# Kernel tuning notes

Measured on AMD Instinct MI355X. Metric: run time of the kernel, lower is better.

Reference implementation:

```python
import jax, jax.numpy as jnp
import numpy as np

HEADS = 8
DIM_HEAD = 64
SCALE = DIM_HEAD ** -0.5


def setup_inputs() -> dict:
    key = jax.random.key(0)
    ks = jax.random.split(key, 6)
    b, n, d = 2, 4096, 1024
    inner = HEADS * DIM_HEAD  # 512
    x = jax.random.normal(ks[0], (b, n, d), dtype=jnp.float32)
    Wq = jax.random.normal(ks[1], (d, inner), dtype=jnp.float32) * (d ** -0.5)
    Wk = jax.random.normal(ks[2], (d, inner), dtype=jnp.float32) * (d ** -0.5)
    Wv = jax.random.normal(ks[3], (d, inner), dtype=jnp.float32) * (d ** -0.5)
    Wout = jax.random.normal(ks[4], (inner, d), dtype=jnp.float32) * (inner ** -0.5)
    bout = jnp.zeros((d,), dtype=jnp.float32)
    return {"x": x, "Wq": Wq, "Wk": Wk, "Wv": Wv, "Wout": Wout, "bout": bout}


def reference(x, Wq, Wk, Wv, Wout, bout):
    b, n, _ = x.shape
    h, dh = HEADS, DIM_HEAD
    # self-attention: context = x
    q = (x @ Wq).reshape(b, n, h, dh).transpose(0, 2, 1, 3)  # b h n d
    k = (x @ Wk).reshape(b, n, h, dh).transpose(0, 2, 1, 3)
    v = (x @ Wv).reshape(b, n, h, dh).transpose(0, 2, 1, 3)
    sim = jnp.einsum('bhid,bhjd->bhij', q, k) * SCALE  # full score matrix
    attn = jax.nn.softmax(sim, axis=-1)
    out = jnp.einsum('bhij,bhjd->bhid', attn, v)
    out = out.transpose(0, 2, 1, 3).reshape(b, n, h * dh)  # b n (h d)
    return out @ Wout + bout
```

## Files before the change

### kernel.cpp

```cpp
#include <hip/hip_runtime.h>
#include <hip/hip_bf16.h>

typedef __bf16 bf16x8 __attribute__((ext_vector_type(8)));
typedef __bf16 bf16x4 __attribute__((ext_vector_type(4)));
typedef float floatx4 __attribute__((ext_vector_type(4)));

#define MFMA16(a, b, c) __builtin_amdgcn_mfma_f32_16x16x32_bf16((a), (b), (c), 0, 0, 0)

__device__ __forceinline__ void stage16(const __bf16* g, __bf16* lds_base) {
  __builtin_amdgcn_global_load_lds(
      (__attribute__((address_space(1))) void*)(void*)g,
      (__attribute__((address_space(3))) void*)lds_base, 16, 0, 0);
}

__global__ void detect_dtype(const unsigned int* __restrict__ x, int* __restrict__ flag) {
  __shared__ int cnt;
  if (threadIdx.x == 0) cnt = 0;
  __syncthreads();
  int c = 0;
  for (int i = threadIdx.x; i < 4096; i += 256) {
    const unsigned f = (x[i] >> 7) & 0xFF;
    c += (f >= 100 && f <= 140) ? 1 : 0;
  }
  atomicAdd(&cnt, c);
  __syncthreads();
  if (threadIdx.x == 0) *flag = (cnt > 2048) ? 1 : 0;
}

__global__ __launch_bounds__(256) void convert_x(const void* __restrict__ src,
                                                 __bf16* __restrict__ dst,
                                                 const int* __restrict__ flagp) {
  const int isbf = *flagp;
  const size_t i = ((size_t)blockIdx.x * 256 + threadIdx.x) * 8;
  if (isbf) {
    *(bf16x8*)(dst + i) = *(const bf16x8*)((const __bf16*)src + i);
  } else {
    const float4 f0 = *(const float4*)((const float*)src + i);
    const float4 f1 = *(const float4*)((const float*)src + i + 4);
    bf16x8 v;
    v[0] = (__bf16)f0.x; v[1] = (__bf16)f0.y; v[2] = (__bf16)f0.z; v[3] = (__bf16)f0.w;
    v[4] = (__bf16)f1.x; v[5] = (__bf16)f1.y; v[6] = (__bf16)f1.z; v[7] = (__bf16)f1.w;
    *(bf16x8*)(dst + i) = v;
  }
}

__global__ __launch_bounds__(256) void transpose3_conv(
    const void* __restrict__ s0, const void* __restrict__ s1,
    const void* __restrict__ s2, __bf16* __restrict__ dst,
    int R, int C, const int* __restrict__ flagp) {
  __shared__ __bf16 t[32][33];
  const int isbf = *flagp;
  const void* src = (blockIdx.z == 0) ? s0 : (blockIdx.z == 1) ? s1 : s2;
  __bf16* d = dst + (size_t)blockIdx.z * R * C;
  const int bx = blockIdx.x * 32, by = blockIdx.y * 32;
  const int x = threadIdx.x & 31, y0 = threadIdx.x >> 5;
#pragma unroll
  for (int i = y0; i < 32; i += 8) {
    const size_t idx = (size_t)(by + i) * C + bx + x;
    t[i][x] = isbf ? ((const __bf16*)src)[idx] : (__bf16)(((const float*)src)[idx]);
  }
  __syncthreads();
#pragma unroll
  for (int i = y0; i < 32; i += 8) d[(size_t)(bx + i) * R + by + x] = t[x][i];
}

__global__ __launch_bounds__(256) void transpose_conv(const void* __restrict__ src,
                                                      __bf16* __restrict__ dst,
                                                      int R, int C,
                                                      const int* __restrict__ flagp) {
  __shared__ __bf16 t[32][33];
  const int isbf = *flagp;
  const int bx = blockIdx.x * 32, by = blockIdx.y * 32;
  const int x = threadIdx.x & 31, y0 = threadIdx.x >> 5;
#pragma unroll
  for (int i = y0; i < 32; i += 8) {
    const size_t idx = (size_t)(by + i) * C + bx + x;
    t[i][x] = isbf ? ((const __bf16*)src)[idx] : (__bf16)(((const float*)src)[idx]);
  }
  __syncthreads();
#pragma unroll
  for (int i = y0; i < 32; i += 8) dst[(size_t)(bx + i) * R + by + x] = t[x][i];
}

__global__ __launch_bounds__(256) void gemm_bt(
    const __bf16* __restrict__ A, const __bf16* __restrict__ Bt,
    void* __restrict__ Cv, void* __restrict__ Cv2, int M, int N, int K,
    const void* __restrict__ bias, int permute, int egress_dual,
    size_t zsC, const int* __restrict__ flagp) {
  __shared__ __attribute__((aligned(16))) __bf16 SH[24576];
  const int isbf = *flagp;
  const int gx = gridDim.x;
  const int nwg = gx * gridDim.y;
  const int orig = blockIdx.x + blockIdx.y * gx;
  const int qq = nwg >> 3;
  const int swz = (orig & 7) * qq + (orig >> 3);
  const int bx = swz % gx, by = swz / gx;

  const int tid = threadIdx.x;
  const int wave = tid >> 6, lane = tid & 63;
  const int m0 = by * 128, n0 = bx * 128;
  const int wm = (wave & 1) * 64, wn = (wave >> 1) * 64;
  const int fr = lane & 15, fq = lane >> 4;

  const floatx4 zero4 = {0.f, 0.f, 0.f, 0.f};
  floatx4 acc[4][4];
#pragma unroll
  for (int i = 0; i < 4; i++)
#pragma unroll
    for (int j = 0; j < 4; j++) acc[i][j] = zero4;

  const int lrow = lane >> 2;
  const int lk = (lane & 3) * 8;
  const int NT = K >> 5;

#pragma unroll
  for (int t0 = 0; t0 < 2; ++t0) {
    const int kk = t0 << 5;
#pragma unroll
    for (int cc = 0; cc < 2; ++cc) {
      const int c = 2 * wave + cc;
      stage16(A + (size_t)(m0 + c * 16 + lrow) * K + kk + lk,
              &SH[t0 * 4096 + c * 512]);
      stage16(Bt + (size_t)(n0 + c * 16 + lrow) * K + kk + lk,
              &SH[12288 + t0 * 4096 + c * 512]);
    }
  }

  for (int t = 0; t < NT; ++t) {
    const int cur = t % 3;
    if (t + 2 < NT) {
      const int sl = (t + 2) % 3;
      const int k2 = (t + 2) << 5;
#pragma unroll
      for (int cc = 0; cc < 2; ++cc) {
        const int c = 2 * wave + cc;
        stage16(A + (size_t)(m0 + c * 16 + lrow) * K + k2 + lk,
                &SH[sl * 4096 + c * 512]);
        stage16(Bt + (size_t)(n0 + c * 16 + lrow) * K + k2 + lk,
                &SH[12288 + sl * 4096 + c * 512]);
      }
      asm volatile("s_waitcnt vmcnt(8)" ::: "memory");
    } else if (t + 1 < NT) {
      asm volatile("s_waitcnt vmcnt(4)" ::: "memory");
    } else {
      asm volatile("s_waitcnt vmcnt(0)" ::: "memory");
    }
    __builtin_amdgcn_s_barrier();
    __builtin_amdgcn_sched_barrier(0);
    bf16x8 af[4], bg[4];
#pragma unroll
    for (int mt = 0; mt < 4; mt++)
      af[mt] = *(const bf16x8*)&SH[cur * 4096 + (wm + mt * 16 + fr) * 32 + fq * 8];
#pragma unroll
    for (int nt = 0; nt < 4; nt++)
      bg[nt] = *(const bf16x8*)&SH[12288 + cur * 4096 + (wn + nt * 16 + fr) * 32 + fq * 8];
#pragma unroll
    for (int mt = 0; mt < 4; mt++)
#pragma unroll
      for (int nt = 0; nt < 4; nt++)
        acc[mt][nt] = MFMA16(af[mt], bg[nt], acc[mt][nt]);
    __builtin_amdgcn_sched_barrier(0);
    __builtin_amdgcn_s_barrier();
  }

  if (permute) {
    const float qs = (n0 < 512) ? 0.18033688011112042f : 1.0f;
#pragma unroll
    for (int mt = 0; mt < 4; mt++)
#pragma unroll
      for (int nt = 0; nt < 4; nt++)
#pragma unroll
        for (int r = 0; r < 4; r++) {
          const int lr = wm + mt * 16 + fq * 4 + r;
          const int lc = wn + nt * 16 + fr;
          SH[lr * 136 + lc] = (__bf16)(acc[mt][nt][r] * qs);
        }
    __syncthreads();
    const int bB = m0 >> 12;
    if (n0 < 1024) {
      const int plane = n0 >> 9;
      const int lr = tid >> 1, ch = (tid & 1) << 6;
      const int col0 = n0 + ch;
      const int bh = bB * 8 + ((col0 & 511) >> 6);
      __bf16* rowp = (__bf16*)Cv + (size_t)plane * zsC + (size_t)bh * 262144 +
                     (size_t)((m0 + lr) & 4095) * 64;
      const __bf16* srcp = &SH[lr * 136 + ch];
#pragma unroll
      for (int k = 0; k < 8; ++k)
        *(bf16x8*)(rowp + k * 8) = *(const bf16x8*)(srcp + k * 8);
    } else {
      const int dloc = tid >> 1, gh = tid & 1;
      const int col0 = n0 + dloc;
      const int bh = bB * 8 + ((col0 & 511) >> 6);
      const int d = col0 & 63;
      __bf16* outp = (__bf16*)Cv2 + (size_t)bh * 262144 + (size_t)d * 4096 +
                     ((m0 & 4095) + (gh << 6));
      const int srow0 = gh << 6;
#pragma unroll
      for (int k = 0; k < 8; ++k) {
        bf16x8 w;
#pragma unroll
        for (int e = 0; e < 8; ++e) {
          const int p = k * 8 + e;
          const int tsrc = ((p & 3) << 4) | (p >> 2);
          w[e] = SH[(srow0 + tsrc) * 136 + dloc];
        }
        *(bf16x8*)(outp + k * 8) = w;
      }
    }
  } else {
#pragma unroll
    for (int mt = 0; mt < 4; mt++)
#pragma unroll
      for (int nt = 0; nt < 4; nt++)
#pragma unroll
        for (int r = 0; r < 4; r++) {
          const int row = m0 + wm + mt * 16 + fq * 4 + r;
          const int col = n0 + wn + nt * 16 + fr;
          float v = acc[mt][nt][r];
          if (bias)
            v += isbf ? (float)((const __bf16*)bias)[col] : ((const float*)bias)[col];
          const size_t idx = (size_t)row * N + col;
          if (egress_dual && !isbf)
            ((float*)Cv)[idx] = v;
          else
            ((__bf16*)Cv)[idx] = (__bf16)v;
        }
  }
}

#define ATT_S 4096
__global__ __launch_bounds__(256, 2) void attn_flash(
    const __bf16* __restrict__ Qa, const __bf16* __restrict__ Ka,
    const __bf16* __restrict__ VPa, __bf16* __restrict__ O) {
  alignas(16) __shared__ __bf16 Kl[3][64 * 64];
  alignas(16) __shared__ __bf16 Vl[3][64 * 64];
  alignas(16) __shared__ __bf16 Pl[4 * 32 * 64];
  const int tid = threadIdx.x, wave = tid >> 6, lane = tid & 63;
  const int orig = blockIdx.x + blockIdx.y * 32;
  const int swz = (orig & 7) * 64 + (orig >> 3);
  const int qx = swz & 31, bh = swz >> 5;
  const int b = bh >> 3, h = bh & 7;
  const int q0 = qx * 128 + wave * 32;
  const int fr = lane & 15, fq = lane >> 4;
  const __bf16* Qb = Qa + (size_t)bh * ATT_S * 64;
  const __bf16* Kb = Ka + (size_t)bh * ATT_S * 64;
  const __bf16* Vb = VPa + (size_t)bh * ATT_S * 64;

  const int sw0 = ((fq ^ (fr & 7)) * 8);
  const int sw1 = (((fq + 4) ^ (fr & 7)) * 8);
  const int r0 = tid >> 3;
  const int ssw = (((tid & 7) ^ (r0 & 7)) * 8);

  bf16x8 aq[2][2];
#pragma unroll
  for (int mt = 0; mt < 2; mt++)
#pragma unroll
    for (int kt = 0; kt < 2; kt++)
      aq[mt][kt] = *(const bf16x8*)(Qb + (size_t)(q0 + mt * 16 + fr) * 64 + kt * 32 + fq * 8);

  const floatx4 zero4 = {0.f, 0.f, 0.f, 0.f};
  floatx4 o[2][4];
  float lsum[2][4];
#pragma unroll
  for (int mt = 0; mt < 2; mt++) {
#pragma unroll
    for (int nt = 0; nt < 4; nt++) o[mt][nt] = zero4;
#pragma unroll
    for (int r = 0; r < 4; r++) lsum[mt][r] = 0.f;
  }

  const int JT = ATT_S / 64;

#pragma unroll
  for (int t0 = 0; t0 < 2; ++t0) {
    const int kv = t0 * 64;
    stage16(Kb + (size_t)(kv + r0) * 64 + ssw, &Kl[t0][wave * 512]);
    stage16(Kb + (size_t)(kv + 32 + r0) * 64 + ssw, &Kl[t0][2048 + wave * 512]);
    stage16(Vb + (size_t)r0 * 4096 + kv + ssw, &Vl[t0][wave * 512]);
    stage16(Vb + (size_t)(32 + r0) * 4096 + kv + ssw, &Vl[t0][2048 + wave * 512]);
  }

  for (int j = 0; j < JT; ++j) {
    const int cur = j % 3;
    if (j + 2 < JT) {
      const int sl = (j + 2) % 3;
      const int kv2 = (j + 2) * 64;
      stage16(Kb + (size_t)(kv2 + r0) * 64 + ssw, &Kl[sl][wave * 512]);
      stage16(Kb + (size_t)(kv2 + 32 + r0) * 64 + ssw, &Kl[sl][2048 + wave * 512]);
      stage16(Vb + (size_t)r0 * 4096 + kv2 + ssw, &Vl[sl][wave * 512]);
      stage16(Vb + (size_t)(32 + r0) * 4096 + kv2 + ssw, &Vl[sl][2048 + wave * 512]);
      asm volatile("s_waitcnt vmcnt(8)" ::: "memory");
    } else if (j + 1 < JT) {
      asm volatile("s_waitcnt vmcnt(4)" ::: "memory");
    } else {
      asm volatile("s_waitcnt vmcnt(0)" ::: "memory");
    }
    __builtin_amdgcn_s_barrier();
    __builtin_amdgcn_sched_barrier(0);
    const __bf16* Klc = Kl[cur];
    const __bf16* Vlc = Vl[cur];

    floatx4 s4[2][4];
    __builtin_amdgcn_s_setprio(1);
#pragma unroll
    for (int nt = 0; nt < 4; nt++) {
      bf16x8 bk0 = *(const bf16x8*)&Klc[(nt * 16 + fr) * 64 + sw0];
      bf16x8 bk1 = *(const bf16x8*)&Klc[(nt * 16 + fr) * 64 + sw1];
#pragma unroll
      for (int mt = 0; mt < 2; mt++) {
        floatx4 zz = zero4;
        zz = MFMA16(aq[mt][0], bk0, zz);
        zz = MFMA16(aq[mt][1], bk1, zz);
        s4[mt][nt] = zz;
      }
    }
    __builtin_amdgcn_s_setprio(0);

#pragma unroll
    for (int mt = 0; mt < 2; mt++)
#pragma unroll
      for (int r = 0; r < 4; r++) {
        bf16x4 pv;
        float psum = 0.f;
#pragma unroll
        for (int nt = 0; nt < 4; nt++) {
          const float p = __builtin_amdgcn_exp2f(s4[mt][nt][r]);
          pv[nt] = (__bf16)p;
          psum += p;
        }
        lsum[mt][r] += psum;
        const int row = wave * 32 + mt * 16 + fq * 4 + r;
        const int vg = (fr >> 1) ^ ((fq * 4 + r) & 7);
        *(bf16x4*)&Pl[row * 64 + vg * 8 + (fr & 1) * 4] = pv;
      }
    asm volatile("s_waitcnt lgkmcnt(0)" ::: "memory");

    bf16x8 bv[4][2];
#pragma unroll
    for (int nt = 0; nt < 4; nt++) {
      bv[nt][0] = *(const bf16x8*)&Vlc[(nt * 16 + fr) * 64 + sw0];
      bv[nt][1] = *(const bf16x8*)&Vlc[(nt * 16 + fr) * 64 + sw1];
    }
    __builtin_amdgcn_s_setprio(1);
#pragma unroll
    for (int mt = 0; mt < 2; mt++) {
      const int prow = (wave * 32 + mt * 16 + fr) * 64;
      bf16x8 ap0 = *(const bf16x8*)&Pl[prow + sw0];
      bf16x8 ap1 = *(const bf16x8*)&Pl[prow + sw1];
#pragma unroll
      for (int nt = 0; nt < 4; nt++) {
        o[mt][nt] = MFMA16(ap0, bv[nt][0], o[mt][nt]);
        o[mt][nt] = MFMA16(ap1, bv[nt][1], o[mt][nt]);
      }
    }
    __builtin_amdgcn_s_setprio(0);
    __builtin_amdgcn_sched_barrier(0);
    __builtin_amdgcn_s_barrier();
  }

#pragma unroll
  for (int off = 1; off < 16; off <<= 1)
#pragma unroll
    for (int mt = 0; mt < 2; mt++)
#pragma unroll
      for (int r = 0; r < 4; r++) lsum[mt][r] += __shfl_xor(lsum[mt][r], off, 64);

#pragma unroll
  for (int mt = 0; mt < 2; mt++)
#pragma unroll
    for (int r = 0; r < 4; r++) {
      const float inv = 1.0f / lsum[mt][r];
      const int row = q0 + mt * 16 + fq * 4 + r;
      __bf16* Orow = O + (size_t)(b * ATT_S + row) * 512 + h * 64;
#pragma unroll
      for (int nt = 0; nt < 4; nt++)
        Orow[nt * 16 + fr] = (__bf16)(o[mt][nt][r] * inv);
    }
}

extern "C" void kernel_launch(void* const* d_in, const int* in_sizes, int n_in,
                              void* d_out, int out_size, void* d_ws, size_t ws_size,
                              hipStream_t stream) {
  (void)in_sizes; (void)n_in; (void)out_size; (void)ws_size;
  const void* x = d_in[0];
  const void* Wq = d_in[1];
  const void* Wk = d_in[2];
  const void* Wv = d_in[3];
  const void* Wout = d_in[4];
  const void* bout = d_in[5];

  char* ws = (char*)d_ws;
  int* flag = (int*)ws;
  __bf16* wtq = (__bf16*)(ws + (1u << 20));
  __bf16* wto = (__bf16*)(ws + (4u << 20));
  __bf16* Q = (__bf16*)(ws + (5u << 20));
  __bf16* K = (__bf16*)(ws + (13u << 20));
  __bf16* VP = (__bf16*)(ws + (21u << 20));
  __bf16* O = (__bf16*)(ws + (29u << 20));
  __bf16* xbf = (__bf16*)(ws + (38u << 20));

  detect_dtype<<<1, 256, 0, stream>>>((const unsigned int*)x, flag);

  transpose3_conv<<<dim3(16, 32, 3), 256, 0, stream>>>(Wq, Wk, Wv, wtq, 1024, 512, flag);
  transpose_conv<<<dim3(32, 16), 256, 0, stream>>>(Wout, wto, 512, 1024, flag);

  convert_x<<<4096, 256, 0, stream>>>(x, xbf, flag);

  gemm_bt<<<dim3(12, 64, 1), 256, 0, stream>>>(
      xbf, wtq, Q, VP, 8192, 1536, 1024, nullptr, 1, 0,
      (size_t)8192 * 512, flag);

  attn_flash<<<dim3(ATT_S / 128, 16), 256, 0, stream>>>(Q, K, VP, O);

  gemm_bt<<<dim3(8, 64, 1), 256, 0, stream>>>(
      O, wto, d_out, nullptr, 8192, 1024, 512, bout, 0, 1, 0, flag);
}
```

Measured before the change: 248.2 us.

## Switch attention to 32x32 MFMA with transposed scores kept in registers

Rewrites the flash-attention inner loop to use 32x32x16 bf16 MFMAs and computes S^T (K as A operand, Q as B operand). The exponentiated probabilities are packed to bf16 and rearranged with cross-half lane shuffles so they can feed the P·V MFMA directly. This removes the P tile's round trip through LDS and its lgkmcnt wait. Row sums are reduced through a small LDS buffer at the end, at the cost of extra packing and shuffle work in registers.

```diff
diff --git a/kernel.cpp b/kernel.cpp
--- a/kernel.cpp
+++ b/kernel.cpp
@@ -4,13 +4,21 @@
 typedef __bf16 bf16x8 __attribute__((ext_vector_type(8)));
 typedef __bf16 bf16x4 __attribute__((ext_vector_type(4)));
 typedef float floatx4 __attribute__((ext_vector_type(4)));
+typedef float floatx16 __attribute__((ext_vector_type(16)));
 
 #define MFMA16(a, b, c) __builtin_amdgcn_mfma_f32_16x16x32_bf16((a), (b), (c), 0, 0, 0)
+#define MFMA32(a, b, c) __builtin_amdgcn_mfma_f32_32x32x16_bf16((a), (b), (c), 0, 0, 0)
 
 __device__ __forceinline__ void stage16(const __bf16* g, __bf16* lds_base) {
   __builtin_amdgcn_global_load_lds(
       (__attribute__((address_space(1))) void*)(void*)g,
       (__attribute__((address_space(3))) void*)lds_base, 16, 0, 0);
+}
+
+__device__ __forceinline__ unsigned pkbf(float lo, float hi) {
+  union { unsigned u; __bf16 h[2]; } w;
+  w.h[0] = (__bf16)lo; w.h[1] = (__bf16)hi;
+  return w.u;
 }
 
 __global__ void detect_dtype(const unsigned int* __restrict__ x, int* __restrict__ flag) {
@@ -235,42 +243,33 @@
     const __bf16* __restrict__ VPa, __bf16* __restrict__ O) {
   alignas(16) __shared__ __bf16 Kl[3][64 * 64];
   alignas(16) __shared__ __bf16 Vl[3][64 * 64];
-  alignas(16) __shared__ __bf16 Pl[4 * 32 * 64];
+  __shared__ float Lw[4][32];
   const int tid = threadIdx.x, wave = tid >> 6, lane = tid & 63;
   const int orig = blockIdx.x + blockIdx.y * 32;
   const int swz = (orig & 7) * 64 + (orig >> 3);
   const int qx = swz & 31, bh = swz >> 5;
   const int b = bh >> 3, h = bh & 7;
   const int q0 = qx * 128 + wave * 32;
-  const int fr = lane & 15, fq = lane >> 4;
+  const int ln = lane & 31, g = lane >> 5;
   const __bf16* Qb = Qa + (size_t)bh * ATT_S * 64;
   const __bf16* Kb = Ka + (size_t)bh * ATT_S * 64;
   const __bf16* Vb = VPa + (size_t)bh * ATT_S * 64;
 
-  const int sw0 = ((fq ^ (fr & 7)) * 8);
-  const int sw1 = (((fq + 4) ^ (fr & 7)) * 8);
   const int r0 = tid >> 3;
   const int ssw = (((tid & 7) ^ (r0 & 7)) * 8);
 
-  bf16x8 aq[2][2];
-#pragma unroll
-  for (int mt = 0; mt < 2; mt++)
-#pragma unroll
-    for (int kt = 0; kt < 2; kt++)
-      aq[mt][kt] = *(const bf16x8*)(Qb + (size_t)(q0 + mt * 16 + fr) * 64 + kt * 32 + fq * 8);
-
-  const floatx4 zero4 = {0.f, 0.f, 0.f, 0.f};
-  floatx4 o[2][4];
-  float lsum[2][4];
-#pragma unroll
-  for (int mt = 0; mt < 2; mt++) {
-#pragma unroll
-    for (int nt = 0; nt < 4; nt++) o[mt][nt] = zero4;
-#pragma unroll
-    for (int r = 0; r < 4; r++) lsum[mt][r] = 0.f;
-  }
+  bf16x8 aq2[4];
+#pragma unroll
+  for (int ds = 0; ds < 4; ds++)
+    aq2[ds] = *(const bf16x8*)(Qb + (size_t)(q0 + ln) * 64 + ds * 16 + g * 8);
+
+  floatx16 o0, o1;
+#pragma unroll
+  for (int r = 0; r < 16; r++) { o0[r] = 0.f; o1[r] = 0.f; }
+  float lsum = 0.f;
 
   const int JT = ATT_S / 64;
+  const int swlo = ln & 7;
 
 #pragma unroll
   for (int t0 = 0; t0 < 2; ++t0) {
@@ -301,82 +300,97 @@
     const __bf16* Klc = Kl[cur];
     const __bf16* Vlc = Vl[cur];
 
-    floatx4 s4[2][4];
+    floatx16 s0, s1;
+#pragma unroll
+    for (int r = 0; r < 16; r++) { s0[r] = 0.f; s1[r] = 0.f; }
     __builtin_amdgcn_s_setprio(1);
 #pragma unroll
-    for (int nt = 0; nt < 4; nt++) {
-      bf16x8 bk0 = *(const bf16x8*)&Klc[(nt * 16 + fr) * 64 + sw0];
-      bf16x8 bk1 = *(const bf16x8*)&Klc[(nt * 16 + fr) * 64 + sw1];
-#pragma unroll
-      for (int mt = 0; mt < 2; mt++) {
-        floatx4 zz = zero4;
-        zz = MFMA16(aq[mt][0], bk0, zz);
-        zz = MFMA16(aq[mt][1], bk1, zz);
-        s4[mt][nt] = zz;
-      }
+    for (int ds = 0; ds < 4; ds++) {
+      const int cg = ds * 2 + g;
+      bf16x8 ak0 = *(const bf16x8*)&Klc[ln * 64 + (cg ^ swlo) * 8];
+      bf16x8 ak1 = *(const bf16x8*)&Klc[(32 + ln) * 64 + (cg ^ swlo) * 8];
+      s0 = MFMA32(ak0, aq2[ds], s0);
+      s1 = MFMA32(ak1, aq2[ds], s1);
     }
     __builtin_amdgcn_s_setprio(0);
 
-#pragma unroll
-    for (int mt = 0; mt < 2; mt++)
-#pragma unroll
-      for (int r = 0; r < 4; r++) {
-        bf16x4 pv;
-        float psum = 0.f;
-#pragma unroll
-        for (int nt = 0; nt < 4; nt++) {
-          const float p = __builtin_amdgcn_exp2f(s4[mt][nt][r]);
-          pv[nt] = (__bf16)p;
-          psum += p;
-        }
-        lsum[mt][r] += psum;
-        const int row = wave * 32 + mt * 16 + fq * 4 + r;
-        const int vg = (fr >> 1) ^ ((fq * 4 + r) & 7);
-        *(bf16x4*)&Pl[row * 64 + vg * 8 + (fr & 1) * 4] = pv;
-      }
-    asm volatile("s_waitcnt lgkmcnt(0)" ::: "memory");
-
-    bf16x8 bv[4][2];
-#pragma unroll
-    for (int nt = 0; nt < 4; nt++) {
-      bv[nt][0] = *(const bf16x8*)&Vlc[(nt * 16 + fr) * 64 + sw0];
-      bv[nt][1] = *(const bf16x8*)&Vlc[(nt * 16 + fr) * 64 + sw1];
-    }
+    float e0[16], e1[16];
+    float ps = 0.f;
+#pragma unroll
+    for (int r = 0; r < 16; r++) {
+      e0[r] = __builtin_amdgcn_exp2f(s0[r]);
+      e1[r] = __builtin_amdgcn_exp2f(s1[r]);
+      ps += e0[r] + e1[r];
+    }
+    lsum += ps;
+
+    unsigned Aw[4] = {pkbf(e0[0], e0[8]),  pkbf(e1[0], e1[8]),
+                      pkbf(e0[1], e0[9]),  pkbf(e1[1], e1[9])};
+    unsigned Bw[4] = {pkbf(e0[2], e0[10]), pkbf(e1[2], e1[10]),
+                      pkbf(e0[3], e0[11]), pkbf(e1[3], e1[11])};
+    unsigned Cw[4] = {pkbf(e0[4], e0[12]), pkbf(e1[4], e1[12]),
+                      pkbf(e0[5], e0[13]), pkbf(e1[5], e1[13])};
+    unsigned Dw[4] = {pkbf(e0[6], e0[14]), pkbf(e1[6], e1[14]),
+                      pkbf(e0[7], e0[15]), pkbf(e1[7], e1[15])};
+    union W8u { unsigned u[4]; bf16x8 v; } fk0, fk1, fk2, fk3;
+#pragma unroll
+    for (int i = 0; i < 4; i++) {
+      const unsigned u1 = g ? Aw[i] : Bw[i];
+      const unsigned r1 = (unsigned)__shfl_xor((int)u1, 32, 64);
+      fk0.u[i] = g ? r1 : Aw[i];
+      fk1.u[i] = g ? Bw[i] : r1;
+      const unsigned u2 = g ? Cw[i] : Dw[i];
+      const unsigned r2 = (unsigned)__shfl_xor((int)u2, 32, 64);
+      fk2.u[i] = g ? r2 : Cw[i];
+      fk3.u[i] = g ? Dw[i] : r2;
+    }
+
     __builtin_amdgcn_s_setprio(1);
-#pragma unroll
-    for (int mt = 0; mt < 2; mt++) {
-      const int prow = (wave * 32 + mt * 16 + fr) * 64;
-      bf16x8 ap0 = *(const bf16x8*)&Pl[prow + sw0];
-      bf16x8 ap1 = *(const bf16x8*)&Pl[prow + sw1];
-#pragma unroll
-      for (int nt = 0; nt < 4; nt++) {
-        o[mt][nt] = MFMA16(ap0, bv[nt][0], o[mt][nt]);
-        o[mt][nt] = MFMA16(ap1, bv[nt][1], o[mt][nt]);
-      }
+    {
+      const int vr = ln;
+      bf16x8 bv0 = *(const bf16x8*)&Vlc[vr * 64 + ((0 + g) ^ swlo) * 8];
+      bf16x8 bv1 = *(const bf16x8*)&Vlc[vr * 64 + ((2 + g) ^ swlo) * 8];
+      bf16x8 bv2 = *(const bf16x8*)&Vlc[vr * 64 + ((4 + g) ^ swlo) * 8];
+      bf16x8 bv3 = *(const bf16x8*)&Vlc[vr * 64 + ((6 + g) ^ swlo) * 8];
+      o0 = MFMA32(fk0.v, bv0, o0);
+      o0 = MFMA32(fk1.v, bv1, o0);
+      o0 = MFMA32(fk2.v, bv2, o0);
+      o0 = MFMA32(fk3.v, bv3, o0);
+    }
+    {
+      const int vr = 32 + ln;
+      bf16x8 bv0 = *(const bf16x8*)&Vlc[vr * 64 + ((0 + g) ^ swlo) * 8];
+      bf16x8 bv1 = *(const bf16x8*)&Vlc[vr * 64 + ((2 + g) ^ swlo) * 8];
+      bf16x8 bv2 = *(const bf16x8*)&Vlc[vr * 64 + ((4 + g) ^ swlo) * 8];
+      bf16x8 bv3 = *(const bf16x8*)&Vlc[vr * 64 + ((6 + g) ^ swlo) * 8];
+      o1 = MFMA32(fk0.v, bv0, o1);
+      o1 = MFMA32(fk1.v, bv1, o1);
+      o1 = MFMA32(fk2.v, bv2, o1);
+      o1 = MFMA32(fk3.v, bv3, o1);
     }
     __builtin_amdgcn_s_setprio(0);
     __builtin_amdgcn_sched_barrier(0);
     __builtin_amdgcn_s_barrier();
   }
 
-#pragma unroll
-  for (int off = 1; off < 16; off <<= 1)
-#pragma unroll
-    for (int mt = 0; mt < 2; mt++)
-#pragma unroll
-      for (int r = 0; r < 4; r++) lsum[mt][r] += __shfl_xor(lsum[mt][r], off, 64);
-
-#pragma unroll
-  for (int mt = 0; mt < 2; mt++)
-#pragma unroll
-    for (int r = 0; r < 4; r++) {
-      const float inv = 1.0f / lsum[mt][r];
-      const int row = q0 + mt * 16 + fq * 4 + r;
-      __bf16* Orow = O + (size_t)(b * ATT_S + row) * 512 + h * 64;
-#pragma unroll
-      for (int nt = 0; nt < 4; nt++)
-        Orow[nt * 16 + fr] = (__bf16)(o[mt][nt][r] * inv);
-    }
+  lsum += __shfl_xor(lsum, 32, 64);
+  if (lane < 32) Lw[wave][lane] = lsum;
+  asm volatile("s_waitcnt lgkmcnt(0)" ::: "memory");
+
+  float inv[16];
+#pragma unroll
+  for (int r = 0; r < 16; r++) {
+    const int q = (r & 3) + 8 * (r >> 2) + 4 * g;
+    inv[r] = 1.0f / Lw[wave][q];
+  }
+#pragma unroll
+  for (int r = 0; r < 16; r++) {
+    const int q = (r & 3) + 8 * (r >> 2) + 4 * g;
+    const int row = q0 + q;
+    __bf16* Orow = O + (size_t)(b * ATT_S + row) * 512 + h * 64;
+    Orow[ln] = (__bf16)(o0[r] * inv[r]);
+    Orow[32 + ln] = (__bf16)(o1[r] * inv[r]);
+  }
 }
 
 extern "C" void kernel_launch(void* const* d_in, const int* in_sizes, int n_in,
```

Result: slower. 265.4 us (+6.9%).
